# Kernel optimization log

Measured on AMD Instinct MI355X. Metric: run time of the kernel, lower is better.

## Reference

```python
import jax, jax.numpy as jnp
import numpy as np

# H36M 17-joint skeleton: parent-of array
_PARENTS = [-1, 0, 1, 2, 0, 4, 5, 0, 7, 8, 9, 8, 11, 12, 8, 14, 15]

def _make_triplets():
    # (jp, j, jc) for every joint j with a parent jp and child jc
    trips = []
    for jc, j in enumerate(_PARENTS):
        if j <= 0 and j != 0:
            continue
        if j == -1:
            continue
        jp = _PARENTS[j]
        if jp == -1:
            continue
        trips.append((jp, j, jc))
    return trips

TRIPLETS = _make_triplets()  # 12 fixed triplets

B, N, J, C = 16, 243, 17, 512
H, D = 8, C // 8
EPS = 1e-5


def setup_inputs() -> dict:
    key = jax.random.key(0)
    ks = jax.random.split(key, 5)
    s = 1.0 / np.sqrt(C)
    x = jax.random.normal(ks[0], (B, N, J, C), dtype=jnp.float32)
    Wqkv = jax.random.normal(ks[1], (C, 3 * C), dtype=jnp.float32) * s
    bqkv = jax.random.normal(ks[2], (3 * C,), dtype=jnp.float32) * 0.01
    Wproj = jax.random.normal(ks[3], (C, C), dtype=jnp.float32) * s
    bproj = jax.random.normal(ks[4], (C,), dtype=jnp.float32) * 0.01
    return {"x": x, "Wqkv": Wqkv, "bqkv": bqkv, "Wproj": Wproj, "bproj": bproj}


def _hsdm(x, Wqkv, bqkv, Wproj, bproj):
    # x: (B, N, J, C) -> tokens over joints per frame
    xf = x.reshape(B * N, J, C)
    qkv = xf @ Wqkv + bqkv                                   # (BN, J, 3C)
    qkv = qkv.reshape(B * N, J, 3, H, D).transpose(2, 0, 3, 1, 4)  # (3, BN, H, J, D)
    q, k, v = qkv[0], qkv[1], qkv[2]
    scale = 1.0 / jnp.sqrt(jnp.float32(D))
    attn = jax.nn.softmax(jnp.einsum('bhqd,bhkd->bhqk', q, k) * scale, axis=-1)
    # sequential hierarchical adjustment over fixed skeleton triplets
    # (order matters: later triplets read entries written by earlier ones)
    for jp, j, jc in TRIPLETS:
        half = attn[:, :, j, jp] * 0.5
        attn = attn.at[:, :, j, jc].add(half).at[:, :, jc, j].add(half)
    # dropout is identity at inference
    xa = jnp.einsum('bhqk,bhkd->bhqd', attn, v)              # (BN, H, J, D)
    xa = xa.transpose(0, 2, 1, 3).reshape(B * N, J, C)
    xa = xa @ Wproj + bproj
    y = x + xa.reshape(B, N, J, C)
    mu = jnp.mean(y, axis=-1, keepdims=True)
    var = jnp.var(y, axis=-1, keepdims=True)
    return (y - mu) / jnp.sqrt(var + EPS)                     # LN without affine


def reference(x, Wqkv, bqkv, Wproj, bproj):
    return _hsdm(x, Wqkv, bqkv, Wproj, bproj)
```

## Files before the change

### kernel.cpp

```cpp
#include <hip/hip_runtime.h>

typedef unsigned short u16;
typedef unsigned int u32;
typedef short bf16x8 __attribute__((ext_vector_type(8)));
typedef float f32x4 __attribute__((ext_vector_type(4)));
typedef float f32x16 __attribute__((ext_vector_type(16)));

#define M_ROWS   66096
#define M_PAD    66176
#define C_DIM    512
#define NQKV     1536
#define NFRAME   3888


__device__ __forceinline__ u16 f2bf(float f) {
    u32 u = __float_as_uint(f);
    u32 r = (u + 0x7fffu + ((u >> 16) & 1u)) >> 16;
    return (u16)r;
}
__device__ __forceinline__ float bf2f(u16 v) {
    return __uint_as_float(((u32)v) << 16);
}
__device__ __forceinline__ void async16(const void* g, void* l) {
    __builtin_amdgcn_global_load_lds(
        (const __attribute__((address_space(1))) unsigned int*)g,
        (__attribute__((address_space(3))) unsigned int*)l, 16, 0, 0);
}


__global__ __launch_bounds__(256) void cast_x(const float* __restrict__ x, u16* __restrict__ xb) {
    u32 cid = blockIdx.x * 256u + threadIdx.x;
    u32 m  = cid >> 6;
    u32 c0 = (cid & 63u) * 8u;
    if (m >= M_PAD) return;
    u16 v[8];
    if (m < M_ROWS) {
        const float* p = x + (size_t)m * C_DIM + c0;
        float4 f1 = *(const float4*)p;
        float4 f2 = *(const float4*)(p + 4);
        v[0]=f2bf(f1.x); v[1]=f2bf(f1.y); v[2]=f2bf(f1.z); v[3]=f2bf(f1.w);
        v[4]=f2bf(f2.x); v[5]=f2bf(f2.y); v[6]=f2bf(f2.z); v[7]=f2bf(f2.w);
    } else {
        #pragma unroll
        for (int i = 0; i < 8; ++i) v[i] = 0;
    }
    u16* dst = xb + ((size_t)(c0 >> 5) * M_PAD + m) * 32 + (c0 & 31u);
    *(uint4*)dst = *(const uint4*)v;
}


__global__ __launch_bounds__(256) void cast_w(const float* __restrict__ W, u16* __restrict__ out, int N) {
    __shared__ float tile[32 * 65];
    const int n0 = blockIdx.x * 64;
    const int kt = blockIdx.y;
    const int t  = threadIdx.x;
    for (int i = t; i < 2048; i += 256) {
        int k = i >> 6, n = i & 63;
        tile[k * 65 + n] = W[(size_t)(kt * 32 + k) * N + n0 + n];
    }
    __syncthreads();
    {
        int n = t >> 2, kk0 = (t & 3) * 8;
        u16 v[8];
        #pragma unroll
        for (int j = 0; j < 8; ++j) v[j] = f2bf(tile[(kk0 + j) * 65 + n]);
        u16* dst = out + ((size_t)kt * N + n0 + n) * 32 + kk0;
        *(uint4*)dst = *(const uint4*)v;
    }
}


__global__ __launch_bounds__(256) void gemm1(const u16* __restrict__ xb,
                                             const u16* __restrict__ wt,
                                             const float* __restrict__ bqkv,
                                             u16* __restrict__ qkv) {
    __shared__ u16 As[2][128 * 32];
    __shared__ u16 Bs[2][128 * 32];
    __shared__ float biasS[128];

    const int n0 = blockIdx.x * 128;
    const int m0 = blockIdx.y * 128;
    const int t  = threadIdx.x;
    const int w  = t >> 6, l = t & 63;
    const int lr = l & 15, lq = l >> 4;
    const int wr = (w >> 1) * 64, wc = (w & 1) * 64;

    if (t < 128) biasS[t] = bqkv[n0 + t];

    f32x4 acc[4][4] = {};

    auto stage = [&](int kt, int bi) {
        const u16* ga = xb + ((size_t)kt * M_PAD + m0) * 32;
        const u16* gb = wt + ((size_t)kt * NQKV + n0) * 32;
        async16(ga + (size_t)t * 8,         &As[bi][t * 8]);
        async16(ga + (size_t)(t + 256) * 8, &As[bi][(t + 256) * 8]);
        async16(gb + (size_t)t * 8,         &Bs[bi][t * 8]);
        async16(gb + (size_t)(t + 256) * 8, &Bs[bi][(t + 256) * 8]);
    };

    stage(0, 0);
    __syncthreads();

    for (int kt = 0; kt < 16; ++kt) {
        const int cur = kt & 1;
        if (kt < 15) stage(kt + 1, cur ^ 1);

        bf16x8 a[4], b[4];
        #pragma unroll
        for (int i = 0; i < 4; ++i) a[i] = *(const bf16x8*)&As[cur][(wr + i * 16 + lr) * 32 + lq * 8];
        #pragma unroll
        for (int i = 0; i < 4; ++i) b[i] = *(const bf16x8*)&Bs[cur][(wc + i * 16 + lr) * 32 + lq * 8];
        #pragma unroll
        for (int i = 0; i < 4; ++i)
            #pragma unroll
            for (int j = 0; j < 4; ++j)
                acc[i][j] = __builtin_amdgcn_mfma_f32_16x16x32_bf16(a[i], b[j], acc[i][j], 0, 0, 0);

        __syncthreads();
    }

    #pragma unroll
    for (int i = 0; i < 4; ++i) {
        #pragma unroll
        for (int j = 0; j < 4; ++j) {
            const int col  = n0 + wc + j * 16 + lr;
            const float bb = biasS[wc + j * 16 + lr];
            #pragma unroll
            for (int r = 0; r < 4; ++r) {
                const int row = m0 + wr + i * 16 + lq * 4 + r;
                if (row < M_ROWS)
                    qkv[(size_t)row * NQKV + col] = f2bf(acc[i][j][r] + bb);
            }
        }
    }
}


__global__ __launch_bounds__(256) void attn_k(const u16* __restrict__ qkv, u16* __restrict__ xa) {
    __shared__ u16 Pb[4][32 * 40];

    const int wv  = threadIdx.x >> 6;
    const int l   = threadIdx.x & 63;
    const int l31 = l & 31;
    const int hi  = l >> 5;

    const int id = blockIdx.x * 4 + wv;
    const int f  = id >> 3;
    const int h  = id & 7;

    const int mrow = (l31 < 17) ? l31 : 0;
    const u16* base = qkv + (size_t)(f * 17) * NQKV;
    const u16* Qp = base + (size_t)mrow * NQKV + h * 64 + 8 * hi;
    const u16* Kp = Qp + 512;

    f32x16 Sacc = {};
    #pragma unroll
    for (int c = 0; c < 4; ++c) {
        bf16x8 aq = *(const bf16x8*)(Qp + 16 * c);
        bf16x8 bk = *(const bf16x8*)(Kp + 16 * c);
        Sacc = __builtin_amdgcn_mfma_f32_32x32x16_bf16(aq, bk, Sacc, 0, 0, 0);
    }

    float p[16];
    #pragma unroll
    for (int r = 0; r < 16; ++r)
        p[r] = (l31 < 17) ? Sacc[r] * 0.125f : -1e30f;

    #pragma unroll
    for (int r = 0; r < 16; ++r) {
        float mx = p[r];
        #pragma unroll
        for (int m = 1; m < 32; m <<= 1) mx = fmaxf(mx, __shfl_xor(mx, m));
        float e = __expf(p[r] - mx);
        float s = e;
        #pragma unroll
        for (int m = 1; m < 32; m <<= 1) s += __shfl_xor(s, m);
        p[r] = e * __builtin_amdgcn_rcpf(s);
    }

    {
        constexpr int TJP[13] = {0,1,0,4,0,7,8,7,8,11,7,8,14};
        constexpr int TJ [13] = {1,2,4,5,7,8,9,8,11,12,8,14,15};
        constexpr int TJC[13] = {2,3,5,6,8,9,10,11,12,13,14,15,16};
        #pragma unroll
        for (int tr = 0; tr < 13; ++tr) {
            const int jp = TJP[tr], j = TJ[tr], jc = TJC[tr];
            const int rj = (j  & 3) | ((j  >> 3) << 2), hj = (j  >> 2) & 1;
            const int rc = (jc & 3) | ((jc >> 3) << 2), hc = (jc >> 2) & 1;
            const float half = 0.5f * __shfl(p[rj], jp + 32 * hj);
            if (l == jc + 32 * hj) p[rj] += half;
            if (l == j  + 32 * hc) p[rc] += half;
        }
    }

    u16* Pw = Pb[wv];
    #pragma unroll
    for (int r = 0; r < 16; ++r) {
        const int row = (r & 3) + 8 * (r >> 2) + 4 * hi;
        Pw[row * 40 + l31] = f2bf(p[r]);
    }
    asm volatile("s_waitcnt lgkmcnt(0)" ::: "memory");

    bf16x8 pa[2];
    #pragma unroll
    for (int c = 0; c < 2; ++c)
        pa[c] = *(const bf16x8*)&Pw[l31 * 40 + 16 * c + 8 * hi];

    const u16* Vbase = base + 1024 + h * 64;
    f32x16 O[2] = {};
    #pragma unroll
    for (int t = 0; t < 2; ++t) {
        #pragma unroll
        for (int c = 0; c < 2; ++c) {
            u16 vv[8];
            #pragma unroll
            for (int j = 0; j < 8; ++j) {
                const int k  = 16 * c + 8 * hi + j;
                const int kr = (k < 17) ? k : 0;
                vv[j] = Vbase[(size_t)kr * NQKV + t * 32 + l31];
            }
            O[t] = __builtin_amdgcn_mfma_f32_32x32x16_bf16(pa[c], *(const bf16x8*)vv, O[t], 0, 0, 0);
        }
    }

    #pragma unroll
    for (int t = 0; t < 2; ++t) {
        const int kt = h * 2 + t;
        #pragma unroll
        for (int r = 0; r < 16; ++r) {
            const int row = (r & 3) + 8 * (r >> 2) + 4 * hi;
            if (row < 17)
                xa[((size_t)kt * M_PAD + (f * 17 + row)) * 32 + l31] = f2bf(O[t][r]);
        }
    }
}


__global__ __launch_bounds__(256) void gemm2_ln(const u16* __restrict__ xa,
                                                const u16* __restrict__ wt,
                                                const float* __restrict__ bproj,
                                                const float* __restrict__ x,
                                                float* __restrict__ out) {
    __shared__ float part[32][4][2];

    const int m0 = blockIdx.x * 32;
    const int t  = threadIdx.x;
    const int wn = t >> 6, l = t & 63;
    const int lr = l & 15, lq = l >> 4;

    f32x4 acc[2][8] = {};

    #pragma unroll 2
    for (int kt = 0; kt < 16; ++kt) {
        const u16* ga = xa + ((size_t)kt * M_PAD + m0 + lr) * 32 + lq * 8;
        const u16* gb = wt + ((size_t)kt * C_DIM + wn * 128 + lr) * 32 + lq * 8;
        bf16x8 a[2], b[8];
        #pragma unroll
        for (int i = 0; i < 2; ++i) a[i] = *(const bf16x8*)(ga + (size_t)i * 16 * 32);
        #pragma unroll
        for (int j = 0; j < 8; ++j) b[j] = *(const bf16x8*)(gb + (size_t)j * 16 * 32);
        #pragma unroll
        for (int i = 0; i < 2; ++i)
            #pragma unroll
            for (int j = 0; j < 8; ++j)
                acc[i][j] = __builtin_amdgcn_mfma_f32_16x16x32_bf16(a[i], b[j], acc[i][j], 0, 0, 0);
    }

    float bias[8];
    #pragma unroll
    for (int j = 0; j < 8; ++j) bias[j] = bproj[wn * 128 + j * 16 + lr];

    float s[2][4], sq[2][4];
    #pragma unroll
    for (int i = 0; i < 2; ++i)
        #pragma unroll
        for (int r = 0; r < 4; ++r) { s[i][r] = 0.f; sq[i][r] = 0.f; }

    #pragma unroll
    for (int i = 0; i < 2; ++i) {
        #pragma unroll
        for (int r = 0; r < 4; ++r) {
            const int rowg = m0 + i * 16 + lq * 4 + r;
            const bool valid = rowg < M_ROWS;
            const float* xr = x + (size_t)rowg * C_DIM + wn * 128 + lr;
            #pragma unroll
            for (int j = 0; j < 8; ++j) {
                float v = acc[i][j][r] + bias[j];
                if (valid) v += xr[j * 16];
                acc[i][j][r] = v;
                s[i][r]  += v;
                sq[i][r] += v * v;
            }
        }
    }

    #pragma unroll
    for (int i = 0; i < 2; ++i)
        #pragma unroll
        for (int r = 0; r < 4; ++r)
            #pragma unroll
            for (int m = 1; m < 16; m <<= 1) {
                s[i][r]  += __shfl_xor(s[i][r],  m);
                sq[i][r] += __shfl_xor(sq[i][r], m);
            }

    if (lr == 0) {
        #pragma unroll
        for (int i = 0; i < 2; ++i)
            #pragma unroll
            for (int r = 0; r < 4; ++r) {
                const int rl = i * 16 + lq * 4 + r;
                part[rl][wn][0] = s[i][r];
                part[rl][wn][1] = sq[i][r];
            }
    }
    __syncthreads();

    #pragma unroll
    for (int i = 0; i < 2; ++i) {
        #pragma unroll
        for (int r = 0; r < 4; ++r) {
            const int rl   = i * 16 + lq * 4 + r;
            const int rowg = m0 + rl;
            const float ss = part[rl][0][0] + part[rl][1][0] + part[rl][2][0] + part[rl][3][0];
            const float qq = part[rl][0][1] + part[rl][1][1] + part[rl][2][1] + part[rl][3][1];
            const float mean = ss * (1.f / 512.f);
            const float var  = qq * (1.f / 512.f) - mean * mean;
            const float rstd = rsqrtf(var + 1e-5f);
            if (rowg < M_ROWS) {
                float* orow = out + (size_t)rowg * C_DIM + wn * 128 + lr;
                #pragma unroll
                for (int j = 0; j < 8; ++j)
                    orow[j * 16] = (acc[i][j][r] - mean) * rstd;
            }
        }
    }
}


extern "C" void kernel_launch(void* const* d_in, const int* in_sizes, int n_in,
                              void* d_out, int out_size, void* d_ws, size_t ws_size,
                              hipStream_t stream) {
    const float* x     = (const float*)d_in[0];
    const float* Wqkv  = (const float*)d_in[1];
    const float* bqkv  = (const float*)d_in[2];
    const float* Wproj = (const float*)d_in[3];
    const float* bproj = (const float*)d_in[4];
    float* out = (float*)d_out;

    u16* xb  = (u16*)d_ws;
    u16* wqt = xb  + (size_t)M_PAD * C_DIM;
    u16* wpt = wqt + (size_t)NQKV * C_DIM;
    u16* qkv = wpt + (size_t)C_DIM * C_DIM;
    u16* xa  = qkv + (size_t)M_PAD * NQKV;

    cast_x<<<(M_PAD * 64) / 256, 256, 0, stream>>>(x, xb);
    cast_w<<<dim3(NQKV / 64, 16), 256, 0, stream>>>(Wqkv, wqt, NQKV);
    cast_w<<<dim3(C_DIM / 64, 16), 256, 0, stream>>>(Wproj, wpt, C_DIM);
    gemm1<<<dim3(NQKV / 128, M_PAD / 128), 256, 0, stream>>>(xb, wqt, bqkv, qkv);
    attn_k<<<(NFRAME * 8) / 4, 256, 0, stream>>>(qkv, xa);
    gemm2_ln<<<(M_ROWS + 31) / 32, 256, 0, stream>>>(xa, wpt, bproj, x, out);
}
```

Baseline: 680.4 us.

## Enlarge gemm2_ln row tile to 128 with 8 waves and register double-buffering

The projection GEMM with fused LayerNorm now processes 128 rows per block with 512 threads. Each of the 8 waves owns 64 output columns, which cuts redundant reloads of the projection weights across blocks. Global loads are double-buffered in registers so the next k-tile's fragments are fetched while the current MFMAs issue. The row statistics are reduced through shared memory across 8 waves with an extra sync, and the larger per-thread accumulator and fragment footprint raises register pressure.

```diff
diff --git a/kernel.cpp b/kernel.cpp
--- a/kernel.cpp
+++ b/kernel.cpp
@@ -236,102 +236,107 @@
 }
 
 
-__global__ __launch_bounds__(256) void gemm2_ln(const u16* __restrict__ xa,
-                                                const u16* __restrict__ wt,
-                                                const float* __restrict__ bproj,
-                                                const float* __restrict__ x,
-                                                float* __restrict__ out) {
-    __shared__ float part[32][4][2];
-
-    const int m0 = blockIdx.x * 32;
+#define G2_LOAD(kt, Af, Bf)                                                          \
+    {                                                                                \
+        const u16* ga = xa + ((size_t)(kt) * M_PAD + m0 + lr) * 32 + lq * 8;         \
+        const u16* gb = wt + ((size_t)(kt) * C_DIM + wn * 64 + lr) * 32 + lq * 8;    \
+        _Pragma("unroll") for (int i = 0; i < 8; ++i)                                \
+            Af[i] = *(const bf16x8*)(ga + (size_t)i * 512);                          \
+        _Pragma("unroll") for (int j = 0; j < 4; ++j)                                \
+            Bf[j] = *(const bf16x8*)(gb + (size_t)j * 512);                          \
+    }
+
+#define G2_MFMA(Af, Bf)                                                              \
+    _Pragma("unroll") for (int i = 0; i < 8; ++i)                                    \
+        _Pragma("unroll") for (int j = 0; j < 4; ++j)                                \
+            acc[i][j] = __builtin_amdgcn_mfma_f32_16x16x32_bf16(Af[i], Bf[j], acc[i][j], 0, 0, 0);
+
+__global__ __launch_bounds__(512, 2) void gemm2_ln(const u16* __restrict__ xa,
+                                                   const u16* __restrict__ wt,
+                                                   const float* __restrict__ bproj,
+                                                   const float* __restrict__ x,
+                                                   float* __restrict__ out) {
+    __shared__ float partS[128][9];
+    __shared__ float partQ[128][9];
+
+    const int m0 = blockIdx.x * 128;
     const int t  = threadIdx.x;
     const int wn = t >> 6, l = t & 63;
     const int lr = l & 15, lq = l >> 4;
 
-    f32x4 acc[2][8] = {};
-
-    #pragma unroll 2
-    for (int kt = 0; kt < 16; ++kt) {
-        const u16* ga = xa + ((size_t)kt * M_PAD + m0 + lr) * 32 + lq * 8;
-        const u16* gb = wt + ((size_t)kt * C_DIM + wn * 128 + lr) * 32 + lq * 8;
-        bf16x8 a[2], b[8];
-        #pragma unroll
-        for (int i = 0; i < 2; ++i) a[i] = *(const bf16x8*)(ga + (size_t)i * 16 * 32);
-        #pragma unroll
-        for (int j = 0; j < 8; ++j) b[j] = *(const bf16x8*)(gb + (size_t)j * 16 * 32);
-        #pragma unroll
-        for (int i = 0; i < 2; ++i)
-            #pragma unroll
-            for (int j = 0; j < 8; ++j)
-                acc[i][j] = __builtin_amdgcn_mfma_f32_16x16x32_bf16(a[i], b[j], acc[i][j], 0, 0, 0);
-    }
-
-    float bias[8];
-    #pragma unroll
-    for (int j = 0; j < 8; ++j) bias[j] = bproj[wn * 128 + j * 16 + lr];
-
-    float s[2][4], sq[2][4];
-    #pragma unroll
-    for (int i = 0; i < 2; ++i)
-        #pragma unroll
-        for (int r = 0; r < 4; ++r) { s[i][r] = 0.f; sq[i][r] = 0.f; }
-
-    #pragma unroll
-    for (int i = 0; i < 2; ++i) {
-        #pragma unroll
-        for (int r = 0; r < 4; ++r) {
-            const int rowg = m0 + i * 16 + lq * 4 + r;
+    f32x4 acc[8][4] = {};
+    bf16x8 A0[8], B0[4], A1[8], B1[4];
+
+    G2_LOAD(0, A0, B0);
+    #pragma unroll 1
+    for (int kt = 0; kt < 14; kt += 2) {
+        G2_LOAD(kt + 1, A1, B1);
+        G2_MFMA(A0, B0);
+        G2_LOAD(kt + 2, A0, B0);
+        G2_MFMA(A1, B1);
+    }
+    G2_LOAD(15, A1, B1);
+    G2_MFMA(A0, B0);
+    G2_MFMA(A1, B1);
+
+    float bias_[4];
+    #pragma unroll
+    for (int j = 0; j < 4; ++j) bias_[j] = bproj[wn * 64 + j * 16 + lr];
+
+    #pragma unroll
+    for (int i = 0; i < 8; ++i) {
+        #pragma unroll
+        for (int rr = 0; rr < 4; ++rr) {
+            const int rl   = i * 16 + lq * 4 + rr;
+            const int rowg = m0 + rl;
             const bool valid = rowg < M_ROWS;
-            const float* xr = x + (size_t)rowg * C_DIM + wn * 128 + lr;
-            #pragma unroll
-            for (int j = 0; j < 8; ++j) {
-                float v = acc[i][j][r] + bias[j];
+            const float* xr = x + (size_t)rowg * C_DIM + wn * 64 + lr;
+            float s = 0.f, q = 0.f;
+            #pragma unroll
+            for (int j = 0; j < 4; ++j) {
+                float v = acc[i][j][rr] + bias_[j];
                 if (valid) v += xr[j * 16];
-                acc[i][j][r] = v;
-                s[i][r]  += v;
-                sq[i][r] += v * v;
-            }
-        }
-    }
-
-    #pragma unroll
-    for (int i = 0; i < 2; ++i)
-        #pragma unroll
-        for (int r = 0; r < 4; ++r)
+                acc[i][j][rr] = v;
+                s += v;
+                q += v * v;
+            }
             #pragma unroll
             for (int m = 1; m < 16; m <<= 1) {
-                s[i][r]  += __shfl_xor(s[i][r],  m);
-                sq[i][r] += __shfl_xor(sq[i][r], m);
-            }
-
-    if (lr == 0) {
-        #pragma unroll
-        for (int i = 0; i < 2; ++i)
-            #pragma unroll
-            for (int r = 0; r < 4; ++r) {
-                const int rl = i * 16 + lq * 4 + r;
-                part[rl][wn][0] = s[i][r];
-                part[rl][wn][1] = sq[i][r];
-            }
+                s += __shfl_xor(s, m);
+                q += __shfl_xor(q, m);
+            }
+            if (lr == 0) {
+                partS[rl][wn] = s;
+                partQ[rl][wn] = q;
+            }
+        }
     }
     __syncthreads();
 
-    #pragma unroll
-    for (int i = 0; i < 2; ++i) {
-        #pragma unroll
-        for (int r = 0; r < 4; ++r) {
-            const int rl   = i * 16 + lq * 4 + r;
+    if (t < 128) {
+        float ss = 0.f, qq = 0.f;
+        #pragma unroll
+        for (int w2 = 0; w2 < 8; ++w2) { ss += partS[t][w2]; qq += partQ[t][w2]; }
+        const float mean = ss * (1.f / 512.f);
+        const float var  = qq * (1.f / 512.f) - mean * mean;
+        partS[t][8] = mean;
+        partQ[t][8] = rsqrtf(var + 1e-5f);
+    }
+    __syncthreads();
+
+    #pragma unroll
+    for (int i = 0; i < 8; ++i) {
+        #pragma unroll
+        for (int rr = 0; rr < 4; ++rr) {
+            const int rl   = i * 16 + lq * 4 + rr;
             const int rowg = m0 + rl;
-            const float ss = part[rl][0][0] + part[rl][1][0] + part[rl][2][0] + part[rl][3][0];
-            const float qq = part[rl][0][1] + part[rl][1][1] + part[rl][2][1] + part[rl][3][1];
-            const float mean = ss * (1.f / 512.f);
-            const float var  = qq * (1.f / 512.f) - mean * mean;
-            const float rstd = rsqrtf(var + 1e-5f);
             if (rowg < M_ROWS) {
-                float* orow = out + (size_t)rowg * C_DIM + wn * 128 + lr;
+                const float mean = partS[rl][8];
+                const float rstd = partQ[rl][8];
+                float* orow = out + (size_t)rowg * C_DIM + wn * 64 + lr;
                 #pragma unroll
-                for (int j = 0; j < 8; ++j)
-                    orow[j * 16] = (acc[i][j][r] - mean) * rstd;
+                for (int j = 0; j < 4; ++j)
+                    orow[j * 16] = (acc[i][j][rr] - mean) * rstd;
             }
         }
     }
@@ -359,5 +364,5 @@
     cast_w<<<dim3(C_DIM / 64, 16), 256, 0, stream>>>(Wproj, wpt, C_DIM);
     gemm1<<<dim3(NQKV / 128, M_PAD / 128), 256, 0, stream>>>(xb, wqt, bqkv, qkv);
     attn_k<<<(NFRAME * 8) / 4, 256, 0, stream>>>(qkv, xa);
-    gemm2_ln<<<(M_ROWS + 31) / 32, 256, 0, stream>>>(xa, wpt, bproj, x, out);
-}
+    gemm2_ln<<<(M_PAD / 128), 512, 0, stream>>>(xa, wpt, bproj, x, out);
+}
```

After: 698.8 us. 1.03x slower.
